# Kernel tuning notes

Hardware: AMD Instinct MI355X
Metric: run time of the kernel (lower is better)

The kernel has to match this reference:

```python
import jax, jax.numpy as jnp
import numpy as np

N, NFEAT, NHID, NHEADS, NCLASS, NBLOCKS = 4096, 1024, 64, 8, 8, 3
ALPHA = 0.1       # LeakyReLU negative slope
NEG = -9e15       # mask value used by pyGAT


def setup_inputs() -> dict:
    key = jax.random.key(0)
    ks = jax.random.split(key, 8)
    x = jax.random.normal(ks[0], (N, NFEAT), jnp.float32)
    # sparse-ish symmetric adjacency with self loops (0/1 int mask)
    a = (jax.random.uniform(ks[1], (N, N)) < 0.01).astype(jnp.int32)
    adj = jnp.maximum(jnp.maximum(a, a.T), jnp.eye(N, dtype=jnp.int32))
    s = 0.1
    W_heads = (jax.random.normal(ks[2], (NHEADS, NFEAT, NHID), jnp.float32) * s)
    a_heads = (jax.random.normal(ks[3], (NHEADS, 2 * NHID), jnp.float32) * s)
    W_out = (jax.random.normal(ks[4], (NHEADS * NHID, NHID), jnp.float32) * s)
    a_out = (jax.random.normal(ks[5], (2 * NHID,), jnp.float32) * s)
    W_gcn = (jax.random.normal(ks[6], (NBLOCKS, NHID, NHID), jnp.float32) * s)
    W_cls = (jax.random.normal(ks[7], (NHID, NCLASS), jnp.float32) * s)
    return dict(x=x, adj=adj, W_heads=W_heads, a_heads=a_heads,
                W_out=W_out, a_out=a_out, W_gcn=W_gcn, W_cls=W_cls)


def _gat_layer(h, mask, W, a, concat):
    # classic pyGAT dense GraphAttentionLayer (inference: dropout off)
    Wh = h @ W                      # [N, nhid]
    nh = Wh.shape[1]
    f1 = Wh @ a[:nh]                # [N]
    f2 = Wh @ a[nh:]                # [N]
    e = jax.nn.leaky_relu(f1[:, None] + f2[None, :], ALPHA)  # [N, N]
    att = jax.nn.softmax(jnp.where(mask, e, NEG), axis=1)
    hp = att @ Wh                   # [N, nhid]
    return jax.nn.elu(hp) if concat else hp


def reference(x, adj, W_heads, a_heads, W_out, a_out, W_gcn, W_cls):
    mask = adj > 0
    # multi-head GAT, concat heads (loop over small fixed head count to keep
    # peak memory at one [N,N] score matrix per step)
    heads = [_gat_layer(x, mask, W_heads[i], a_heads[i], True)
             for i in range(NHEADS)]
    h = jnp.concatenate(heads, axis=1)           # [N, nheads*nhid]
    h = _gat_layer(h, mask, W_out, a_out, False)  # [N, nhid]
    # ModifiedGCN: symmetric-normalized dense propagation, n_blocks + head
    af = adj.astype(h.dtype)
    dinv = jax.lax.rsqrt(jnp.sum(af, axis=1))
    a_norm = af * dinv[:, None] * dinv[None, :]   # D^-1/2 A D^-1/2
    for i in range(NBLOCKS):
        h = jax.nn.relu(a_norm @ (h @ W_gcn[i]))
    return a_norm @ (h @ W_cls)                   # [N, nclass]
```

## Files before the change

### kernel.cpp

```cpp
#include <hip/hip_runtime.h>
#include <hip/hip_bf16.h>
#include <math.h>

#define N_NODES 4096
#define NFEAT   1024
#define NHEADS  8
#define ALPHA   0.1f
#define MAXDEG  256

typedef short short8 __attribute__((ext_vector_type(8)));
typedef float f32x4  __attribute__((ext_vector_type(4)));

__device__ __forceinline__ ushort f2bf(float f) {
    uint b = __float_as_uint(f);
    b += 0x7FFFu + ((b >> 16) & 1u);
    return (ushort)(b >> 16);
}
__device__ __forceinline__ float bf2f(ushort u) {
    return __uint_as_float(((uint)u) << 16);
}

__global__ __launch_bounds__(256) void prep_all(const float* __restrict__ x,
                                                const int* __restrict__ adj,
                                                const float* __restrict__ Whd,
                                                const float* __restrict__ Wo,
                                                short* __restrict__ x3,
                                                short* __restrict__ W3,
                                                short* __restrict__ W23,
                                                ushort* __restrict__ csr,
                                                int* __restrict__ rowlen,
                                                float* __restrict__ dinv) {
    __shared__ float tile[64][65];
    int b = blockIdx.x, t = threadIdx.x;
    if (b < 4096) {
        size_t idx = ((size_t)b * 256 + t) * 4;
        int row = (int)(idx >> 10);
        int col = (int)(idx & 1023);
        float4 v = *(const float4*)(x + idx);
        ushort h0 = f2bf(v.x), h1 = f2bf(v.y), h2 = f2bf(v.z), h3 = f2bf(v.w);
        short4 h = make_short4((short)h0, (short)h1, (short)h2, (short)h3);
        short4 l = make_short4((short)f2bf(v.x - bf2f(h0)), (short)f2bf(v.y - bf2f(h1)),
                               (short)f2bf(v.z - bf2f(h2)), (short)f2bf(v.w - bf2f(h3)));
        short* rp = x3 + (size_t)row * 3072 + col;
        *(short4*)(rp)        = h;
        *(short4*)(rp + 1024) = l;
        *(short4*)(rp + 2048) = h;
        return;
    }
    if (b < 4232) {
        const float* W; short* B3; int K, head, kb;
        if (b < 4224) { int id = b - 4096; W = Whd; B3 = W3;  K = 1024; head = id >> 4; kb = id & 15; }
        else          { int id = b - 4224; W = Wo;  B3 = W23; K = 512;  head = 0;       kb = id; }
        int k0 = kb * 64;
        const float* src = W + (size_t)head * K * 64 + (size_t)k0 * 64;
#pragma unroll
        for (int i = 0; i < 16; i++) {
            int lin = t + i * 256;
            int kk = lin >> 6, nn = lin & 63;
            tile[nn][kk] = src[kk * 64 + nn];
        }
        __syncthreads();
#pragma unroll
        for (int i = 0; i < 16; i++) {
            int lin = t + i * 256;
            int nn = lin >> 6, kk = lin & 63;
            float v = tile[nn][kk];
            ushort h = f2bf(v);
            ushort l = f2bf(v - bf2f(h));
            short* rp = B3 + (size_t)(head * 64 + nn) * (3 * (size_t)K) + k0 + kk;
            rp[0]     = (short)h;
            rp[K]     = (short)h;
            rp[2 * K] = (short)l;
        }
        return;
    }
    int wid = t >> 6, lane = t & 63;
    int row = (b - 4232) * 4 + wid;
    const int4* arow = (const int4*)(adj + (size_t)row * N_NODES);
    unsigned long long pre = (1ull << lane) - 1ull;
    int count = 0;
    ushort* crow = csr + (size_t)row * MAXDEG;
    for (int blk = 0; blk < N_NODES / 256; blk++) {
        int4 v = arow[blk * 64 + lane];
        unsigned long long m0 = __ballot(v.x != 0);
        unsigned long long m1 = __ballot(v.y != 0);
        unsigned long long m2 = __ballot(v.z != 0);
        unsigned long long m3 = __ballot(v.w != 0);
        int pos = count + __popcll(m0 & pre) + __popcll(m1 & pre)
                        + __popcll(m2 & pre) + __popcll(m3 & pre);
        int base = blk * 256 + lane * 4;
        if (v.x) { if (pos < MAXDEG) crow[pos] = (ushort)base;       pos++; }
        if (v.y) { if (pos < MAXDEG) crow[pos] = (ushort)(base + 1); pos++; }
        if (v.z) { if (pos < MAXDEG) crow[pos] = (ushort)(base + 2); pos++; }
        if (v.w) { if (pos < MAXDEG) crow[pos] = (ushort)(base + 3); pos++; }
        count += __popcll(m0) + __popcll(m1) + __popcll(m2) + __popcll(m3);
    }
    if (lane == 0) {
        rowlen[row] = count < MAXDEG ? count : MAXDEG;
        dinv[row] = 1.0f / sqrtf((float)count);
    }
}

#define GBM 64
#define GBN 64
#define GBK 64
#define LDK 72

__global__ __launch_bounds__(256, 2) void gemm_mfma(const short* __restrict__ A,
                                                    const short* __restrict__ B,
                                                    float* __restrict__ C,
                                                    int Kp, int kChunk, int cPartStride,
                                                    int swz, int headmajor,
                                                    const float* __restrict__ aH,
                                                    float* __restrict__ f1h,
                                                    float* __restrict__ f2h) {
    __shared__ __align__(16) short As[2][GBM * LDK];
    __shared__ __align__(16) short Bs[2][GBN * LDK];

    int tid = threadIdx.x, lane = tid & 63, wid = tid >> 6;
    int wr = wid >> 1, wc = wid & 1;
    int bx, by;
    if (swz) {
        int lin = blockIdx.x;
        bx = (lin & 7) * 8 + (lin >> 6);
        by = (lin >> 3) & 7;
    } else {
        bx = blockIdx.x; by = blockIdx.y;
    }
    int row0 = bx * GBM, col0 = by * GBN;
    int kbase = blockIdx.z * kChunk;
    C += (size_t)blockIdx.z * cPartStride;

    int aRow[2], aKc[2], bRow[2], bKc[2];
#pragma unroll
    for (int c = 0; c < 2; c++) {
        int lin = tid + c * 256;
        aRow[c] = lin >> 3; aKc[c] = (lin & 7) * 8;
        bRow[c] = lin >> 3; bKc[c] = (lin & 7) * 8;
    }

    short8 rA[2], rB[2];
    auto LOAD = [&](int k0) {
#pragma unroll
        for (int c = 0; c < 2; c++) {
            rA[c] = *(const short8*)(A + (size_t)(row0 + aRow[c]) * Kp + kbase + k0 + aKc[c]);
            rB[c] = *(const short8*)(B + (size_t)(col0 + bRow[c]) * Kp + kbase + k0 + bKc[c]);
        }
    };
    auto WRITE = [&](int buf) {
#pragma unroll
        for (int c = 0; c < 2; c++) {
            *(short8*)&As[buf][aRow[c] * LDK + aKc[c]] = rA[c];
            *(short8*)&Bs[buf][bRow[c] * LDK + bKc[c]] = rB[c];
        }
    };

    f32x4 acc[2][2];
#pragma unroll
    for (int m = 0; m < 2; m++)
#pragma unroll
        for (int n = 0; n < 2; n++) acc[m][n] = (f32x4){0.f, 0.f, 0.f, 0.f};

    LOAD(0);
    WRITE(0);
    __syncthreads();

    int nt = kChunk / GBK;
    for (int t = 0; t < nt; ++t) {
        int cur = t & 1;
        if (t + 1 < nt) LOAD((t + 1) * GBK);
#pragma unroll
        for (int ks = 0; ks < 2; ++ks) {
            short8 ah[2], bh[2];
            int ko = ks * 32 + (lane >> 4) * 8;
#pragma unroll
            for (int m = 0; m < 2; m++)
                ah[m] = *(const short8*)&As[cur][(wr * 32 + m * 16 + (lane & 15)) * LDK + ko];
#pragma unroll
            for (int n = 0; n < 2; n++)
                bh[n] = *(const short8*)&Bs[cur][(wc * 32 + n * 16 + (lane & 15)) * LDK + ko];
#pragma unroll
            for (int m = 0; m < 2; m++)
#pragma unroll
                for (int n = 0; n < 2; n++)
                    acc[m][n] = __builtin_amdgcn_mfma_f32_16x16x32_bf16(ah[m], bh[n], acc[m][n], 0, 0, 0);
        }
        if (t + 1 < nt) WRITE(cur ^ 1);
        __syncthreads();
    }

#pragma unroll
    for (int m = 0; m < 2; m++)
#pragma unroll
        for (int n = 0; n < 2; n++)
#pragma unroll
            for (int r = 0; r < 4; r++) {
                int rr = row0 + wr * 32 + m * 16 + (lane >> 4) * 4 + r;
                int cc = col0 + wc * 32 + n * 16 + (lane & 15);
                if (headmajor)
                    C[(size_t)(cc >> 6) * (N_NODES * 64) + (size_t)rr * 64 + (cc & 63)] = acc[m][n][r];
                else
                    C[(size_t)rr * 64 + cc] = acc[m][n][r];
            }

    if (aH) {
        __shared__ float f1p[2][64], f2p[2][64];
        const float* ahp = aH + by * 128;
        int cl = lane & 15;
        float a1x = ahp[wc * 32 + cl],      a1y = ahp[wc * 32 + 16 + cl];
        float a2x = ahp[64 + wc * 32 + cl], a2y = ahp[64 + wc * 32 + 16 + cl];
#pragma unroll
        for (int m = 0; m < 2; m++)
#pragma unroll
            for (int r = 0; r < 4; r++) {
                float s1 = acc[m][0][r] * a1x + acc[m][1][r] * a1y;
                float s2 = acc[m][0][r] * a2x + acc[m][1][r] * a2y;
#pragma unroll
                for (int off = 1; off < 16; off <<= 1) {
                    s1 += __shfl_xor(s1, off);
                    s2 += __shfl_xor(s2, off);
                }
                if ((lane & 15) == 0) {
                    int rl = wr * 32 + m * 16 + (lane >> 4) * 4 + r;
                    f1p[wc][rl] = s1;
                    f2p[wc][rl] = s2;
                }
            }
        __syncthreads();
        if (tid < 64) {
            f1h[(size_t)by * N_NODES + row0 + tid] = f1p[0][tid] + f1p[1][tid];
            f2h[(size_t)by * N_NODES + row0 + tid] = f2p[0][tid] + f2p[1][tid];
        }
    }
}

__global__ __launch_bounds__(512, 8) void attn1(const float* __restrict__ Whh,
                                                const float* __restrict__ f1h,
                                                const float* __restrict__ f2h,
                                                const ushort* __restrict__ csr,
                                                const int* __restrict__ rowlen,
                                                short* __restrict__ hp3) {
    __shared__ float  f2s[N_NODES];
    __shared__ float  w[8][MAXDEG];
    __shared__ ushort cols[8][MAXDEG];
    int lin = blockIdx.x;
    int h = lin & 7;
    int wid = threadIdx.x >> 6, lane = threadIdx.x & 63;
    int i = (lin >> 3) * 8 + wid;

    {
        const float4* f2g = (const float4*)(f2h + (size_t)h * N_NODES);
        float4 v0 = f2g[threadIdx.x];
        float4 v1 = f2g[threadIdx.x + 512];
        *(float4*)&f2s[threadIdx.x * 4] = v0;
        *(float4*)&f2s[(threadIdx.x + 512) * 4] = v1;
    }
    __syncthreads();

    int len = rowlen[i];
    const ushort* crow = csr + (size_t)i * MAXDEG;
    float f1v = f1h[(size_t)h * N_NODES + i];

    float ev[4]; int cv[4];
    float m = -1e30f;
#pragma unroll
    for (int c = 0; c < 4; c++) {
        int k = lane + c * 64;
        if (k < len) {
            int j = crow[k];
            float e = f1v + f2s[j];
            e = e > 0.f ? e : ALPHA * e;
            ev[c] = e; cv[c] = j;
            m = fmaxf(m, e);
        }
    }
#pragma unroll
    for (int off = 32; off; off >>= 1) m = fmaxf(m, __shfl_xor(m, off));
    float s = 0.f;
#pragma unroll
    for (int c = 0; c < 4; c++) {
        int k = lane + c * 64;
        if (k < len) {
            float ex = __expf(ev[c] - m);
            s += ex;
            w[wid][k] = ex;
            cols[wid][k] = (ushort)cv[c];
        }
    }
#pragma unroll
    for (int off = 32; off; off >>= 1) s += __shfl_xor(s, off);
    float sinv = 1.0f / s;

    int len16 = (len + 15) & ~15;
    if (lane < len16 - len) {
        w[wid][len + lane] = 0.f;
        cols[wid][len + lane] = 0;
    }

    int q = lane >> 4, d = lane & 15;
    const float4* base = (const float4*)(Whh + (size_t)h * (N_NODES * 64)) + d;
    f32x4 A0 = {0.f,0.f,0.f,0.f}, A1 = A0, A2 = A0, A3 = A0;
    for (int k = 0; k < len16; k += 16) {
        int   j0 = cols[wid][k + q];       float w0 = w[wid][k + q];
        int   j1 = cols[wid][k + 4 + q];   float w1 = w[wid][k + 4 + q];
        int   j2 = cols[wid][k + 8 + q];   float w2 = w[wid][k + 8 + q];
        int   j3 = cols[wid][k + 12 + q];  float w3 = w[wid][k + 12 + q];
        float4 v0 = base[(size_t)j0 * 16];
        float4 v1 = base[(size_t)j1 * 16];
        float4 v2 = base[(size_t)j2 * 16];
        float4 v3 = base[(size_t)j3 * 16];
        A0[0] += w0 * v0.x; A0[1] += w0 * v0.y; A0[2] += w0 * v0.z; A0[3] += w0 * v0.w;
        A1[0] += w1 * v1.x; A1[1] += w1 * v1.y; A1[2] += w1 * v1.z; A1[3] += w1 * v1.w;
        A2[0] += w2 * v2.x; A2[1] += w2 * v2.y; A2[2] += w2 * v2.z; A2[3] += w2 * v2.w;
        A3[0] += w3 * v3.x; A3[1] += w3 * v3.y; A3[2] += w3 * v3.z; A3[3] += w3 * v3.w;
    }
    float rx = (A0[0] + A1[0]) + (A2[0] + A3[0]);
    float ry = (A0[1] + A1[1]) + (A2[1] + A3[1]);
    float rz = (A0[2] + A1[2]) + (A2[2] + A3[2]);
    float rw = (A0[3] + A1[3]) + (A2[3] + A3[3]);
#pragma unroll
    for (int off = 16; off <= 32; off <<= 1) {
        rx += __shfl_xor(rx, off);
        ry += __shfl_xor(ry, off);
        rz += __shfl_xor(rz, off);
        rw += __shfl_xor(rw, off);
    }
    if (lane < 16) {
        float v[4] = {rx * sinv, ry * sinv, rz * sinv, rw * sinv};
        short hi[4], lo[4];
#pragma unroll
        for (int c = 0; c < 4; c++) {
            float e = v[c] > 0.f ? v[c] : __expf(v[c]) - 1.f;
            ushort hh = f2bf(e);
            hi[c] = (short)hh;
            lo[c] = (short)f2bf(e - bf2f(hh));
        }
        short* rp = hp3 + (size_t)i * 1536 + h * 64 + d * 4;
        *(short4*)(rp)        = make_short4(hi[0], hi[1], hi[2], hi[3]);
        *(short4*)(rp + 512)  = make_short4(lo[0], lo[1], lo[2], lo[3]);
        *(short4*)(rp + 1024) = make_short4(hi[0], hi[1], hi[2], hi[3]);
    }
}

__global__ __launch_bounds__(256) void f2sum(const float* __restrict__ part,
                                             const float* __restrict__ a,
                                             float* __restrict__ Wh2,
                                             float* __restrict__ f1o,
                                             float* __restrict__ f2o) {
    int wid = threadIdx.x >> 6, l = threadIdx.x & 63;
    int i = blockIdx.x * 4 + wid;
    size_t o = (size_t)i * 64 + l;
    const size_t S = (size_t)N_NODES * 64;
    float v = part[o] + part[o + S] + part[o + 2 * S] + part[o + 3 * S];
    Wh2[o] = v;
    float p1 = v * a[l], p2 = v * a[64 + l];
#pragma unroll
    for (int off = 32; off; off >>= 1) {
        p1 += __shfl_xor(p1, off);
        p2 += __shfl_xor(p2, off);
    }
    if (l == 0) { f1o[i] = p1; f2o[i] = p2; }
}

__global__ __launch_bounds__(256, 6) void attn2_g0(const float* __restrict__ Wh2,
                                                   const float* __restrict__ f1o,
                                                   const float* __restrict__ f2o,
                                                   const ushort* __restrict__ csr,
                                                   const int* __restrict__ rowlen,
                                                   const float* __restrict__ W0,
                                                   const float* __restrict__ dinv,
                                                   float* __restrict__ t0) {
    __shared__ float  f2s[N_NODES];
    __shared__ float  w[4][MAXDEG];
    __shared__ ushort cl[4][MAXDEG];
    __shared__ float  hrow[4][64];
    int wid = threadIdx.x >> 6, lane = threadIdx.x & 63;
    int i = blockIdx.x * 4 + wid;

    {
        const float4* f2g = (const float4*)f2o;
#pragma unroll
        for (int c = 0; c < 4; c++) {
            int idx = threadIdx.x + c * 256;
            *(float4*)&f2s[idx * 4] = f2g[idx];
        }
    }
    __syncthreads();

    int len = rowlen[i];
    const ushort* crow = csr + (size_t)i * MAXDEG;
    float myf1 = f1o[i];

    float ev[4]; int cv[4];
    float m = -1e30f;
#pragma unroll
    for (int c = 0; c < 4; c++) {
        int k = lane + c * 64;
        if (k < len) {
            int j = crow[k];
            float e = myf1 + f2s[j];
            e = e > 0.f ? e : ALPHA * e;
            ev[c] = e; cv[c] = j;
            m = fmaxf(m, e);
        }
    }
#pragma unroll
    for (int off = 32; off; off >>= 1) m = fmaxf(m, __shfl_xor(m, off));
    float s = 0.f;
#pragma unroll
    for (int c = 0; c < 4; c++) {
        int k = lane + c * 64;
        if (k < len) {
            float ex = __expf(ev[c] - m);
            s += ex;
            w[wid][k] = ex;
            cl[wid][k] = (ushort)cv[c];
        }
    }
#pragma unroll
    for (int off = 32; off; off >>= 1) s += __shfl_xor(s, off);
    float sinv = 1.0f / s;

    int len16 = (len + 15) & ~15;
    if (lane < len16 - len) {
        w[wid][len + lane] = 0.f;
        cl[wid][len + lane] = 0;
    }

    int q = lane >> 4, d = lane & 15;
    const float4* base = (const float4*)Wh2 + d;
    f32x4 A0 = {0.f,0.f,0.f,0.f}, A1 = A0, A2 = A0, A3 = A0;
    for (int k = 0; k < len16; k += 16) {
        int   j0 = cl[wid][k + q];       float w0 = w[wid][k + q];
        int   j1 = cl[wid][k + 4 + q];   float w1 = w[wid][k + 4 + q];
        int   j2 = cl[wid][k + 8 + q];   float w2 = w[wid][k + 8 + q];
        int   j3 = cl[wid][k + 12 + q];  float w3 = w[wid][k + 12 + q];
        float4 v0 = base[(size_t)j0 * 16];
        float4 v1 = base[(size_t)j1 * 16];
        float4 v2 = base[(size_t)j2 * 16];
        float4 v3 = base[(size_t)j3 * 16];
        A0[0] += w0 * v0.x; A0[1] += w0 * v0.y; A0[2] += w0 * v0.z; A0[3] += w0 * v0.w;
        A1[0] += w1 * v1.x; A1[1] += w1 * v1.y; A1[2] += w1 * v1.z; A1[3] += w1 * v1.w;
        A2[0] += w2 * v2.x; A2[1] += w2 * v2.y; A2[2] += w2 * v2.z; A2[3] += w2 * v2.w;
        A3[0] += w3 * v3.x; A3[1] += w3 * v3.y; A3[2] += w3 * v3.z; A3[3] += w3 * v3.w;
    }
    float rx = (A0[0] + A1[0]) + (A2[0] + A3[0]);
    float ry = (A0[1] + A1[1]) + (A2[1] + A3[1]);
    float rz = (A0[2] + A1[2]) + (A2[2] + A3[2]);
    float rw = (A0[3] + A1[3]) + (A2[3] + A3[3]);
#pragma unroll
    for (int off = 16; off <= 32; off <<= 1) {
        rx += __shfl_xor(rx, off);
        ry += __shfl_xor(ry, off);
        rz += __shfl_xor(rz, off);
        rw += __shfl_xor(rw, off);
    }
    if (lane < 16) {
        float4 r = make_float4(rx * sinv, ry * sinv, rz * sinv, rw * sinv);
        *(float4*)&hrow[wid][d * 4] = r;
    }

    float ox = 0.f, oy = 0.f, oz = 0.f, ow = 0.f;
#pragma unroll
    for (int it = 0; it < 16; it++) {
        int kk = q * 16 + it;
        float hv = hrow[wid][kk];
        float4 wv = *(const float4*)(W0 + kk * 64 + d * 4);
        ox += hv * wv.x; oy += hv * wv.y; oz += hv * wv.z; ow += hv * wv.w;
    }
#pragma unroll
    for (int off = 16; off <= 32; off <<= 1) {
        ox += __shfl_xor(ox, off);
        oy += __shfl_xor(oy, off);
        oz += __shfl_xor(oz, off);
        ow += __shfl_xor(ow, off);
    }
    if (lane < 16) {
        float di = dinv[i];
        *(float4*)(t0 + (size_t)i * 64 + d * 4) =
            make_float4(ox * di, oy * di, oz * di, ow * di);
    }
}

__global__ __launch_bounds__(256, 4) void spmv_gemm(const float* __restrict__ t,
                                                    const ushort* __restrict__ csr,
                                                    const int* __restrict__ rowlen,
                                                    const float* __restrict__ W,
                                                    const float* __restrict__ dinv,
                                                    float* __restrict__ out) {
    __shared__ float hrow[4][64];
    int wid = threadIdx.x >> 6, lane = threadIdx.x & 63;
    int i = blockIdx.x * 4 + wid;
    int len = rowlen[i];
    const ushort* ci = csr + (size_t)i * MAXDEG;
    int q = lane >> 4, d = lane & 15;
    const float4* base = (const float4*)t + d;
    int len16 = (len + 15) & ~15;
    f32x4 A0 = {0.f,0.f,0.f,0.f}, A1 = A0, A2 = A0, A3 = A0;
    for (int k = 0; k < len16; k += 16) {
        int k0 = k + q, k1 = k + 4 + q, k2 = k + 8 + q, k3 = k + 12 + q;
        float m0 = k0 < len ? 1.f : 0.f;
        float m1 = k1 < len ? 1.f : 0.f;
        float m2 = k2 < len ? 1.f : 0.f;
        float m3 = k3 < len ? 1.f : 0.f;
        int j0 = ci[k0 < len ? k0 : 0];
        int j1 = ci[k1 < len ? k1 : 0];
        int j2 = ci[k2 < len ? k2 : 0];
        int j3 = ci[k3 < len ? k3 : 0];
        float4 v0 = base[(size_t)j0 * 16];
        float4 v1 = base[(size_t)j1 * 16];
        float4 v2 = base[(size_t)j2 * 16];
        float4 v3 = base[(size_t)j3 * 16];
        A0[0] += m0 * v0.x; A0[1] += m0 * v0.y; A0[2] += m0 * v0.z; A0[3] += m0 * v0.w;
        A1[0] += m1 * v1.x; A1[1] += m1 * v1.y; A1[2] += m1 * v1.z; A1[3] += m1 * v1.w;
        A2[0] += m2 * v2.x; A2[1] += m2 * v2.y; A2[2] += m2 * v2.z; A2[3] += m2 * v2.w;
        A3[0] += m3 * v3.x; A3[1] += m3 * v3.y; A3[2] += m3 * v3.z; A3[3] += m3 * v3.w;
    }
    float rx = (A0[0] + A1[0]) + (A2[0] + A3[0]);
    float ry = (A0[1] + A1[1]) + (A2[1] + A3[1]);
    float rz = (A0[2] + A1[2]) + (A2[2] + A3[2]);
    float rw = (A0[3] + A1[3]) + (A2[3] + A3[3]);
#pragma unroll
    for (int off = 16; off <= 32; off <<= 1) {
        rx += __shfl_xor(rx, off);
        ry += __shfl_xor(ry, off);
        rz += __shfl_xor(rz, off);
        rw += __shfl_xor(rw, off);
    }
    float di = dinv[i];
    if (lane < 16) {
        float4 r = make_float4(fmaxf(rx * di, 0.f), fmaxf(ry * di, 0.f),
                               fmaxf(rz * di, 0.f), fmaxf(rw * di, 0.f));
        *(float4*)&hrow[wid][d * 4] = r;
    }

    float ox = 0.f, oy = 0.f, oz = 0.f, ow = 0.f;
#pragma unroll
    for (int it = 0; it < 16; it++) {
        int kk = q * 16 + it;
        float hv = hrow[wid][kk];
        float4 wv = *(const float4*)(W + kk * 64 + d * 4);
        ox += hv * wv.x; oy += hv * wv.y; oz += hv * wv.z; ow += hv * wv.w;
    }
#pragma unroll
    for (int off = 16; off <= 32; off <<= 1) {
        ox += __shfl_xor(ox, off);
        oy += __shfl_xor(oy, off);
        oz += __shfl_xor(oz, off);
        ow += __shfl_xor(ow, off);
    }
    if (lane < 16)
        *(float4*)(out + (size_t)i * 64 + d * 4) =
            make_float4(ox * di, oy * di, oz * di, ow * di);
}

__global__ __launch_bounds__(256, 4) void spmv_cls(const float* __restrict__ t,
                                                   const ushort* __restrict__ csr,
                                                   const int* __restrict__ rowlen,
                                                   const float* __restrict__ Wc,
                                                   const float* __restrict__ dinv,
                                                   float* __restrict__ t8) {
    __shared__ float hrow[4][64];
    int wid = threadIdx.x >> 6, lane = threadIdx.x & 63;
    int i = blockIdx.x * 4 + wid;
    int len = rowlen[i];
    const ushort* ci = csr + (size_t)i * MAXDEG;
    int q = lane >> 4, d = lane & 15;
    const float4* base = (const float4*)t + d;
    int len16 = (len + 15) & ~15;
    f32x4 A0 = {0.f,0.f,0.f,0.f}, A1 = A0, A2 = A0, A3 = A0;
    for (int k = 0; k < len16; k += 16) {
        int k0 = k + q, k1 = k + 4 + q, k2 = k + 8 + q, k3 = k + 12 + q;
        float m0 = k0 < len ? 1.f : 0.f;
        float m1 = k1 < len ? 1.f : 0.f;
        float m2 = k2 < len ? 1.f : 0.f;
        float m3 = k3 < len ? 1.f : 0.f;
        int j0 = ci[k0 < len ? k0 : 0];
        int j1 = ci[k1 < len ? k1 : 0];
        int j2 = ci[k2 < len ? k2 : 0];
        int j3 = ci[k3 < len ? k3 : 0];
        float4 v0 = base[(size_t)j0 * 16];
        float4 v1 = base[(size_t)j1 * 16];
        float4 v2 = base[(size_t)j2 * 16];
        float4 v3 = base[(size_t)j3 * 16];
        A0[0] += m0 * v0.x; A0[1] += m0 * v0.y; A0[2] += m0 * v0.z; A0[3] += m0 * v0.w;
        A1[0] += m1 * v1.x; A1[1] += m1 * v1.y; A1[2] += m1 * v1.z; A1[3] += m1 * v1.w;
        A2[0] += m2 * v2.x; A2[1] += m2 * v2.y; A2[2] += m2 * v2.z; A2[3] += m2 * v2.w;
        A3[0] += m3 * v3.x; A3[1] += m3 * v3.y; A3[2] += m3 * v3.z; A3[3] += m3 * v3.w;
    }
    float rx = (A0[0] + A1[0]) + (A2[0] + A3[0]);
    float ry = (A0[1] + A1[1]) + (A2[1] + A3[1]);
    float rz = (A0[2] + A1[2]) + (A2[2] + A3[2]);
    float rw = (A0[3] + A1[3]) + (A2[3] + A3[3]);
#pragma unroll
    for (int off = 16; off <= 32; off <<= 1) {
        rx += __shfl_xor(rx, off);
        ry += __shfl_xor(ry, off);
        rz += __shfl_xor(rz, off);
        rw += __shfl_xor(rw, off);
    }
    float di = dinv[i];
    if (lane < 16) {
        float4 r = make_float4(fmaxf(rx * di, 0.f), fmaxf(ry * di, 0.f),
                               fmaxf(rz * di, 0.f), fmaxf(rw * di, 0.f));
        *(float4*)&hrow[wid][d * 4] = r;
    }
    int col = lane & 7, k0s = (lane >> 3) * 8;
    float o = 0.f;
#pragma unroll
    for (int kk = 0; kk < 8; kk++) o += hrow[wid][k0s + kk] * Wc[(k0s + kk) * 8 + col];
    o += __shfl_down(o, 32);
    o += __shfl_down(o, 16);
    o += __shfl_down(o, 8);
    if (lane < 8) t8[(size_t)i * 8 + lane] = o * di;
}

__global__ __launch_bounds__(256) void spmv8(const float* __restrict__ t8,
                                             const ushort* __restrict__ csr,
                                             const int* __restrict__ rowlen,
                                             const float* __restrict__ dinv,
                                             float* __restrict__ out) {
    int wid = threadIdx.x >> 6, lane = threadIdx.x & 63;
    int i = blockIdx.x * 4 + wid;
    int len = rowlen[i];
    const ushort* ci = csr + (size_t)i * MAXDEG;
    int col = lane & 7, chunk = lane >> 3;
    float acc = 0.f;
    for (int k = chunk; k < len; k += 8)
        acc += t8[(size_t)ci[k] * 8 + col];
    acc += __shfl_down(acc, 32);
    acc += __shfl_down(acc, 16);
    acc += __shfl_down(acc, 8);
    if (lane < 8) out[(size_t)i * 8 + lane] = acc * dinv[i];
}

extern "C" void kernel_launch(void* const* d_in, const int* in_sizes, int n_in,
                              void* d_out, int out_size, void* d_ws, size_t ws_size,
                              hipStream_t stream) {
    const float* x       = (const float*)d_in[0];
    const int*   adj     = (const int*)d_in[1];
    const float* W_heads = (const float*)d_in[2];
    const float* a_heads = (const float*)d_in[3];
    const float* W_out   = (const float*)d_in[4];
    const float* a_out   = (const float*)d_in[5];
    const float* W_gcn   = (const float*)d_in[6];
    const float* W_cls   = (const float*)d_in[7];
    float* outp = (float*)d_out;

    char* p = (char*)d_ws;
    short*  x3     = (short*)p;  p += (size_t)N_NODES * 3072 * 2;
    short*  W3     = (short*)p;  p += (size_t)512 * 3072 * 2;
    short*  W23    = (short*)p;  p += (size_t)64 * 1536 * 2;
    float*  Whh    = (float*)p;  p += (size_t)NHEADS * N_NODES * 64 * 4;
    float*  f1h    = (float*)p;  p += (size_t)NHEADS * N_NODES * 4;
    float*  f2h    = (float*)p;  p += (size_t)NHEADS * N_NODES * 4;
    float*  Wh2    = (float*)p;  p += (size_t)N_NODES * 64 * 4;
    float*  f1o    = (float*)p;  p += (size_t)N_NODES * 4;
    float*  f2o    = (float*)p;  p += (size_t)N_NODES * 4;
    float*  tA     = (float*)p;  p += (size_t)N_NODES * 64 * 4;
    float*  tB     = (float*)p;  p += (size_t)N_NODES * 64 * 4;
    float*  t8     = (float*)p;  p += (size_t)N_NODES * 8 * 4;
    float*  dinv   = (float*)p;  p += (size_t)N_NODES * 4;
    int*    rowlen = (int*)p;    p += (size_t)N_NODES * 4;
    ushort* csr    = (ushort*)p; p += (size_t)N_NODES * MAXDEG * 2;

    short* hp3  = x3;
    float* part = (float*)((char*)x3 + (16u << 20));

    prep_all<<<4096 + 128 + 8 + 1024, 256, 0, stream>>>(
        x, adj, W_heads, W_out, x3, W3, W23, csr, rowlen, dinv);

    gemm_mfma<<<512, 256, 0, stream>>>(x3, W3, Whh, 3072, 3072, 0, 1, 1,
                                       a_heads, f1h, f2h);

    attn1<<<N_NODES * NHEADS / 8, 512, 0, stream>>>(Whh, f1h, f2h, csr, rowlen, hp3);

    gemm_mfma<<<dim3(N_NODES / GBM, 1, 4), 256, 0, stream>>>(
        hp3, W23, part, 1536, 384, N_NODES * 64, 0, 0, nullptr, nullptr, nullptr);

    f2sum<<<N_NODES / 4, 256, 0, stream>>>(part, a_out, Wh2, f1o, f2o);

    attn2_g0<<<N_NODES / 4, 256, 0, stream>>>(Wh2, f1o, f2o, csr, rowlen, W_gcn, dinv, tA);

    spmv_gemm<<<N_NODES / 4, 256, 0, stream>>>(tA, csr, rowlen, W_gcn + 4096, dinv, tB);
    spmv_gemm<<<N_NODES / 4, 256, 0, stream>>>(tB, csr, rowlen, W_gcn + 8192, dinv, tA);

    spmv_cls<<<N_NODES / 4, 256, 0, stream>>>(tA, csr, rowlen, W_cls, dinv, t8);
    spmv8<<<N_NODES / 4, 256, 0, stream>>>(t8, csr, rowlen, dinv, outp);
}
```

Before: 245.1 us.

## Deepen GEMM K tile and software-pipeline gather loops in attention and SpMV kernels

The MFMA GEMM K tile doubles from 64 to 128 (LDS stride 136), so each thread loads four 16-byte chunks per operand and there are fewer barrier-separated iterations. The gather loops in attn1, the second attention kernel and spmv_gemm are software-pipelined: the next 16 neighbour rows are prefetched into registers while the current ones are accumulated. The last prefetch reads index 0 harmlessly. Launch-bound occupancy hints change (attn1 8→6, spmv_gemm 4→6). This trades more registers and LDS for better latency hiding.

```diff
diff --git a/kernel.cpp b/kernel.cpp
--- a/kernel.cpp
+++ b/kernel.cpp
@@ -103,8 +103,8 @@
 
 #define GBM 64
 #define GBN 64
-#define GBK 64
-#define LDK 72
+#define GBK 128
+#define LDK 136
 
 __global__ __launch_bounds__(256, 2) void gemm_mfma(const short* __restrict__ A,
                                                     const short* __restrict__ B,
@@ -131,27 +131,26 @@
     int kbase = blockIdx.z * kChunk;
     C += (size_t)blockIdx.z * cPartStride;
 
-    int aRow[2], aKc[2], bRow[2], bKc[2];
-#pragma unroll
-    for (int c = 0; c < 2; c++) {
+    int aRow[4], aKc[4];
+#pragma unroll
+    for (int c = 0; c < 4; c++) {
         int lin = tid + c * 256;
-        aRow[c] = lin >> 3; aKc[c] = (lin & 7) * 8;
-        bRow[c] = lin >> 3; bKc[c] = (lin & 7) * 8;
-    }
-
-    short8 rA[2], rB[2];
+        aRow[c] = lin >> 4; aKc[c] = (lin & 15) * 8;
+    }
+
+    short8 rA[4], rB[4];
     auto LOAD = [&](int k0) {
 #pragma unroll
-        for (int c = 0; c < 2; c++) {
+        for (int c = 0; c < 4; c++) {
             rA[c] = *(const short8*)(A + (size_t)(row0 + aRow[c]) * Kp + kbase + k0 + aKc[c]);
-            rB[c] = *(const short8*)(B + (size_t)(col0 + bRow[c]) * Kp + kbase + k0 + bKc[c]);
+            rB[c] = *(const short8*)(B + (size_t)(col0 + aRow[c]) * Kp + kbase + k0 + aKc[c]);
         }
     };
     auto WRITE = [&](int buf) {
 #pragma unroll
-        for (int c = 0; c < 2; c++) {
+        for (int c = 0; c < 4; c++) {
             *(short8*)&As[buf][aRow[c] * LDK + aKc[c]] = rA[c];
-            *(short8*)&Bs[buf][bRow[c] * LDK + bKc[c]] = rB[c];
+            *(short8*)&Bs[buf][aRow[c] * LDK + aKc[c]] = rB[c];
         }
     };
 
@@ -170,7 +169,7 @@
         int cur = t & 1;
         if (t + 1 < nt) LOAD((t + 1) * GBK);
 #pragma unroll
-        for (int ks = 0; ks < 2; ++ks) {
+        for (int ks = 0; ks < GBK / 32; ++ks) {
             short8 ah[2], bh[2];
             int ko = ks * 32 + (lane >> 4) * 8;
 #pragma unroll
@@ -234,7 +233,7 @@
     }
 }
 
-__global__ __launch_bounds__(512, 8) void attn1(const float* __restrict__ Whh,
+__global__ __launch_bounds__(512, 6) void attn1(const float* __restrict__ Whh,
                                                 const float* __restrict__ f1h,
                                                 const float* __restrict__ f2h,
                                                 const ushort* __restrict__ csr,
@@ -300,20 +299,36 @@
     int q = lane >> 4, d = lane & 15;
     const float4* base = (const float4*)(Whh + (size_t)h * (N_NODES * 64)) + d;
     f32x4 A0 = {0.f,0.f,0.f,0.f}, A1 = A0, A2 = A0, A3 = A0;
-    for (int k = 0; k < len16; k += 16) {
-        int   j0 = cols[wid][k + q];       float w0 = w[wid][k + q];
-        int   j1 = cols[wid][k + 4 + q];   float w1 = w[wid][k + 4 + q];
-        int   j2 = cols[wid][k + 8 + q];   float w2 = w[wid][k + 8 + q];
-        int   j3 = cols[wid][k + 12 + q];  float w3 = w[wid][k + 12 + q];
-        float4 v0 = base[(size_t)j0 * 16];
-        float4 v1 = base[(size_t)j1 * 16];
-        float4 v2 = base[(size_t)j2 * 16];
-        float4 v3 = base[(size_t)j3 * 16];
+
+    int   j0 = cols[wid][q],      j1 = cols[wid][4 + q];
+    int   j2 = cols[wid][8 + q],  j3 = cols[wid][12 + q];
+    float w0 = w[wid][q],         w1 = w[wid][4 + q];
+    float w2 = w[wid][8 + q],     w3 = w[wid][12 + q];
+    float4 v0 = base[(size_t)j0 * 16];
+    float4 v1 = base[(size_t)j1 * 16];
+    float4 v2 = base[(size_t)j2 * 16];
+    float4 v3 = base[(size_t)j3 * 16];
+
+    for (int k = 16; k <= len16; k += 16) {
+        int kk = (k < len16) ? k : 0;
+        int   n0 = cols[wid][kk + q],      n1 = cols[wid][kk + 4 + q];
+        int   n2 = cols[wid][kk + 8 + q],  n3 = cols[wid][kk + 12 + q];
+        float u0 = w[wid][kk + q],         u1 = w[wid][kk + 4 + q];
+        float u2 = w[wid][kk + 8 + q],     u3 = w[wid][kk + 12 + q];
+        float4 p0 = base[(size_t)n0 * 16];
+        float4 p1 = base[(size_t)n1 * 16];
+        float4 p2 = base[(size_t)n2 * 16];
+        float4 p3 = base[(size_t)n3 * 16];
+
         A0[0] += w0 * v0.x; A0[1] += w0 * v0.y; A0[2] += w0 * v0.z; A0[3] += w0 * v0.w;
         A1[0] += w1 * v1.x; A1[1] += w1 * v1.y; A1[2] += w1 * v1.z; A1[3] += w1 * v1.w;
         A2[0] += w2 * v2.x; A2[1] += w2 * v2.y; A2[2] += w2 * v2.z; A2[3] += w2 * v2.w;
         A3[0] += w3 * v3.x; A3[1] += w3 * v3.y; A3[2] += w3 * v3.z; A3[3] += w3 * v3.w;
-    }
+
+        w0 = u0; w1 = u1; w2 = u2; w3 = u3;
+        v0 = p0; v1 = p1; v2 = p2; v3 = p3;
+    }
+
     float rx = (A0[0] + A1[0]) + (A2[0] + A3[0]);
     float ry = (A0[1] + A1[1]) + (A2[1] + A3[1]);
     float rz = (A0[2] + A1[2]) + (A2[2] + A3[2]);
@@ -430,19 +445,34 @@
     int q = lane >> 4, d = lane & 15;
     const float4* base = (const float4*)Wh2 + d;
     f32x4 A0 = {0.f,0.f,0.f,0.f}, A1 = A0, A2 = A0, A3 = A0;
-    for (int k = 0; k < len16; k += 16) {
-        int   j0 = cl[wid][k + q];       float w0 = w[wid][k + q];
-        int   j1 = cl[wid][k + 4 + q];   float w1 = w[wid][k + 4 + q];
-        int   j2 = cl[wid][k + 8 + q];   float w2 = w[wid][k + 8 + q];
-        int   j3 = cl[wid][k + 12 + q];  float w3 = w[wid][k + 12 + q];
-        float4 v0 = base[(size_t)j0 * 16];
-        float4 v1 = base[(size_t)j1 * 16];
-        float4 v2 = base[(size_t)j2 * 16];
-        float4 v3 = base[(size_t)j3 * 16];
+
+    int   j0 = cl[wid][q],      j1 = cl[wid][4 + q];
+    int   j2 = cl[wid][8 + q],  j3 = cl[wid][12 + q];
+    float w0 = w[wid][q],       w1 = w[wid][4 + q];
+    float w2 = w[wid][8 + q],   w3 = w[wid][12 + q];
+    float4 v0 = base[(size_t)j0 * 16];
+    float4 v1 = base[(size_t)j1 * 16];
+    float4 v2 = base[(size_t)j2 * 16];
+    float4 v3 = base[(size_t)j3 * 16];
+
+    for (int k = 16; k <= len16; k += 16) {
+        int kk = (k < len16) ? k : 0;
+        int   n0 = cl[wid][kk + q],      n1 = cl[wid][kk + 4 + q];
+        int   n2 = cl[wid][kk + 8 + q],  n3 = cl[wid][kk + 12 + q];
+        float u0 = w[wid][kk + q],       u1 = w[wid][kk + 4 + q];
+        float u2 = w[wid][kk + 8 + q],   u3 = w[wid][kk + 12 + q];
+        float4 p0 = base[(size_t)n0 * 16];
+        float4 p1 = base[(size_t)n1 * 16];
+        float4 p2 = base[(size_t)n2 * 16];
+        float4 p3 = base[(size_t)n3 * 16];
+
         A0[0] += w0 * v0.x; A0[1] += w0 * v0.y; A0[2] += w0 * v0.z; A0[3] += w0 * v0.w;
         A1[0] += w1 * v1.x; A1[1] += w1 * v1.y; A1[2] += w1 * v1.z; A1[3] += w1 * v1.w;
         A2[0] += w2 * v2.x; A2[1] += w2 * v2.y; A2[2] += w2 * v2.z; A2[3] += w2 * v2.w;
         A3[0] += w3 * v3.x; A3[1] += w3 * v3.y; A3[2] += w3 * v3.z; A3[3] += w3 * v3.w;
+
+        w0 = u0; w1 = u1; w2 = u2; w3 = u3;
+        v0 = p0; v1 = p1; v2 = p2; v3 = p3;
     }
     float rx = (A0[0] + A1[0]) + (A2[0] + A3[0]);
     float ry = (A0[1] + A1[1]) + (A2[1] + A3[1]);
@@ -482,7 +512,7 @@
     }
 }
 
-__global__ __launch_bounds__(256, 4) void spmv_gemm(const float* __restrict__ t,
+__global__ __launch_bounds__(256, 6) void spmv_gemm(const float* __restrict__ t,
                                                     const ushort* __restrict__ csr,
                                                     const int* __restrict__ rowlen,
                                                     const float* __restrict__ W,
@@ -497,24 +527,44 @@
     const float4* base = (const float4*)t + d;
     int len16 = (len + 15) & ~15;
     f32x4 A0 = {0.f,0.f,0.f,0.f}, A1 = A0, A2 = A0, A3 = A0;
-    for (int k = 0; k < len16; k += 16) {
-        int k0 = k + q, k1 = k + 4 + q, k2 = k + 8 + q, k3 = k + 12 + q;
-        float m0 = k0 < len ? 1.f : 0.f;
-        float m1 = k1 < len ? 1.f : 0.f;
-        float m2 = k2 < len ? 1.f : 0.f;
-        float m3 = k3 < len ? 1.f : 0.f;
-        int j0 = ci[k0 < len ? k0 : 0];
-        int j1 = ci[k1 < len ? k1 : 0];
-        int j2 = ci[k2 < len ? k2 : 0];
-        int j3 = ci[k3 < len ? k3 : 0];
-        float4 v0 = base[(size_t)j0 * 16];
-        float4 v1 = base[(size_t)j1 * 16];
-        float4 v2 = base[(size_t)j2 * 16];
-        float4 v3 = base[(size_t)j3 * 16];
-        A0[0] += m0 * v0.x; A0[1] += m0 * v0.y; A0[2] += m0 * v0.z; A0[3] += m0 * v0.w;
-        A1[0] += m1 * v1.x; A1[1] += m1 * v1.y; A1[2] += m1 * v1.z; A1[3] += m1 * v1.w;
-        A2[0] += m2 * v2.x; A2[1] += m2 * v2.y; A2[2] += m2 * v2.z; A2[3] += m2 * v2.w;
-        A3[0] += m3 * v3.x; A3[1] += m3 * v3.y; A3[2] += m3 * v3.z; A3[3] += m3 * v3.w;
+
+    int k0 = q, k1 = 4 + q, k2 = 8 + q, k3 = 12 + q;
+    float w0 = k0 < len ? 1.f : 0.f;
+    float w1 = k1 < len ? 1.f : 0.f;
+    float w2 = k2 < len ? 1.f : 0.f;
+    float w3 = k3 < len ? 1.f : 0.f;
+    int j0 = ci[k0 < len ? k0 : 0];
+    int j1 = ci[k1 < len ? k1 : 0];
+    int j2 = ci[k2 < len ? k2 : 0];
+    int j3 = ci[k3 < len ? k3 : 0];
+    float4 v0 = base[(size_t)j0 * 16];
+    float4 v1 = base[(size_t)j1 * 16];
+    float4 v2 = base[(size_t)j2 * 16];
+    float4 v3 = base[(size_t)j3 * 16];
+
+    for (int k = 16; k <= len16; k += 16) {
+        int kk = (k < len16) ? k : 0;
+        int K0 = kk + q, K1 = kk + 4 + q, K2 = kk + 8 + q, K3 = kk + 12 + q;
+        float u0 = K0 < len ? 1.f : 0.f;
+        float u1 = K1 < len ? 1.f : 0.f;
+        float u2 = K2 < len ? 1.f : 0.f;
+        float u3 = K3 < len ? 1.f : 0.f;
+        int n0 = ci[K0 < len ? K0 : 0];
+        int n1 = ci[K1 < len ? K1 : 0];
+        int n2 = ci[K2 < len ? K2 : 0];
+        int n3 = ci[K3 < len ? K3 : 0];
+        float4 p0 = base[(size_t)n0 * 16];
+        float4 p1 = base[(size_t)n1 * 16];
+        float4 p2 = base[(size_t)n2 * 16];
+        float4 p3 = base[(size_t)n3 * 16];
+
+        A0[0] += w0 * v0.x; A0[1] += w0 * v0.y; A0[2] += w0 * v0.z; A0[3] += w0 * v0.w;
+        A1[0] += w1 * v1.x; A1[1] += w1 * v1.y; A1[2] += w1 * v1.z; A1[3] += w1 * v1.w;
+        A2[0] += w2 * v2.x; A2[1] += w2 * v2.y; A2[2] += w2 * v2.z; A2[3] += w2 * v2.w;
+        A3[0] += w3 * v3.x; A3[1] += w3 * v3.y; A3[2] += w3 * v3.z; A3[3] += w3 * v3.w;
+
+        w0 = u0; w1 = u1; w2 = u2; w3 = u3;
+        v0 = p0; v1 = p1; v2 = p2; v3 = p3;
     }
     float rx = (A0[0] + A1[0]) + (A2[0] + A3[0]);
     float ry = (A0[1] + A1[1]) + (A2[1] + A3[1]);
```

Measured after the change: 243.3 us. Within noise of the previous version (-0.8%).

## Add dedicated 128-row GEMM with direct LDS loads, two rows per wave in attn1

Applied to the files above, without the earlier changes.

Adds a dedicated first-layer GEMM with 128x64 tiles. It stages A and B straight into LDS with global_load_lds and keeps the fused f1/f2 attention projection epilogue. The generic gemm_mfma loses its head-major and fused-projection paths and moves to a K tile of 128 (LDK 136) for the second GEMM. attn1 now processes two rows per wave with 8-wide padding, and spmv_gemm's launch bound moves to 6 waves. The aim is more reuse per tile, fewer register round-trips for staging, and more memory-level parallelism in the gather. The cost is higher LDS use, which may lower occupancy, especially in attn1.

```diff
diff --git a/kernel.cpp b/kernel.cpp
--- a/kernel.cpp
+++ b/kernel.cpp
@@ -101,57 +101,155 @@
     }
 }
 
+__global__ __launch_bounds__(256) void gemm1_m97(const short* __restrict__ A,
+                                                 const short* __restrict__ B,
+                                                 float* __restrict__ C,
+                                                 const float* __restrict__ aH,
+                                                 float* __restrict__ f1h,
+                                                 float* __restrict__ f2h) {
+    __shared__ __align__(16) short As[2][128 * 64];
+    __shared__ __align__(16) short Bs[2][64 * 64];
+    __shared__ float f1p[2][128], f2p[2][128];
+
+    int tid = threadIdx.x, lane = tid & 63, wid = tid >> 6;
+    int wr = wid >> 1, wc = wid & 1;
+    int lin = blockIdx.x;
+    int bx = (lin & 7) * 4 + (lin >> 6);
+    int by = (lin >> 3) & 7;
+    int row0 = bx * 128, col0 = by * 64;
+    const int Kp = 3072;
+
+    int sRow = lane >> 3;
+    int sCol = (lane & 7) * 8;
+
+    auto STAGE = [&](int buf, int k0) {
+#pragma unroll
+        for (int c = 0; c < 4; c++) {
+            int q = c * 4 + wid;
+            const short* gp = A + (size_t)(row0 + 8 * q + sRow) * Kp + k0 + sCol;
+            __builtin_amdgcn_global_load_lds(
+                (const __attribute__((address_space(1))) void*)gp,
+                (__attribute__((address_space(3))) void*)&As[buf][q * 512], 16, 0, 0);
+        }
+#pragma unroll
+        for (int c = 0; c < 2; c++) {
+            int q = c * 4 + wid;
+            const short* gp = B + (size_t)(col0 + 8 * q + sRow) * Kp + k0 + sCol;
+            __builtin_amdgcn_global_load_lds(
+                (const __attribute__((address_space(1))) void*)gp,
+                (__attribute__((address_space(3))) void*)&Bs[buf][q * 512], 16, 0, 0);
+        }
+    };
+
+    f32x4 acc[4][2];
+#pragma unroll
+    for (int m = 0; m < 4; m++)
+#pragma unroll
+        for (int n = 0; n < 2; n++) acc[m][n] = (f32x4){0.f, 0.f, 0.f, 0.f};
+
+    STAGE(0, 0);
+    __syncthreads();
+
+    const int nt = 48;
+    for (int t = 0; t < nt; ++t) {
+        int cur = t & 1;
+        if (t + 1 < nt) STAGE(cur ^ 1, (t + 1) * 64);
+#pragma unroll
+        for (int ks = 0; ks < 2; ++ks) {
+            short8 ah[4], bh[2];
+            int ko = ks * 32 + (lane >> 4) * 8;
+#pragma unroll
+            for (int m = 0; m < 4; m++)
+                ah[m] = *(const short8*)&As[cur][(wr * 64 + m * 16 + (lane & 15)) * 64 + ko];
+#pragma unroll
+            for (int n = 0; n < 2; n++)
+                bh[n] = *(const short8*)&Bs[cur][(wc * 32 + n * 16 + (lane & 15)) * 64 + ko];
+#pragma unroll
+            for (int m = 0; m < 4; m++)
+#pragma unroll
+                for (int n = 0; n < 2; n++)
+                    acc[m][n] = __builtin_amdgcn_mfma_f32_16x16x32_bf16(ah[m], bh[n], acc[m][n], 0, 0, 0);
+        }
+        __syncthreads();
+    }
+
+#pragma unroll
+    for (int m = 0; m < 4; m++)
+#pragma unroll
+        for (int n = 0; n < 2; n++)
+#pragma unroll
+            for (int r = 0; r < 4; r++) {
+                int rr = row0 + wr * 64 + m * 16 + (lane >> 4) * 4 + r;
+                int cc = wc * 32 + n * 16 + (lane & 15);
+                C[(size_t)by * (N_NODES * 64) + (size_t)rr * 64 + cc] = acc[m][n][r];
+            }
+
+    const float* ahp = aH + by * 128;
+    int cl = lane & 15;
+    float a1x = ahp[wc * 32 + cl],      a1y = ahp[wc * 32 + 16 + cl];
+    float a2x = ahp[64 + wc * 32 + cl], a2y = ahp[64 + wc * 32 + 16 + cl];
+#pragma unroll
+    for (int m = 0; m < 4; m++)
+#pragma unroll
+        for (int r = 0; r < 4; r++) {
+            float s1 = acc[m][0][r] * a1x + acc[m][1][r] * a1y;
+            float s2 = acc[m][0][r] * a2x + acc[m][1][r] * a2y;
+#pragma unroll
+            for (int off = 1; off < 16; off <<= 1) {
+                s1 += __shfl_xor(s1, off);
+                s2 += __shfl_xor(s2, off);
+            }
+            if ((lane & 15) == 0) {
+                int rl = wr * 64 + m * 16 + (lane >> 4) * 4 + r;
+                f1p[wc][rl] = s1;
+                f2p[wc][rl] = s2;
+            }
+        }
+    __syncthreads();
+    if (tid < 128) {
+        f1h[(size_t)by * N_NODES + row0 + tid] = f1p[0][tid] + f1p[1][tid];
+        f2h[(size_t)by * N_NODES + row0 + tid] = f2p[0][tid] + f2p[1][tid];
+    }
+}
+
 #define GBM 64
 #define GBN 64
-#define GBK 64
-#define LDK 72
+#define GBK 128
+#define LDK 136
 
 __global__ __launch_bounds__(256, 2) void gemm_mfma(const short* __restrict__ A,
                                                     const short* __restrict__ B,
                                                     float* __restrict__ C,
-                                                    int Kp, int kChunk, int cPartStride,
-                                                    int swz, int headmajor,
-                                                    const float* __restrict__ aH,
-                                                    float* __restrict__ f1h,
-                                                    float* __restrict__ f2h) {
+                                                    int Kp, int kChunk, int cPartStride) {
     __shared__ __align__(16) short As[2][GBM * LDK];
     __shared__ __align__(16) short Bs[2][GBN * LDK];
 
     int tid = threadIdx.x, lane = tid & 63, wid = tid >> 6;
     int wr = wid >> 1, wc = wid & 1;
-    int bx, by;
-    if (swz) {
-        int lin = blockIdx.x;
-        bx = (lin & 7) * 8 + (lin >> 6);
-        by = (lin >> 3) & 7;
-    } else {
-        bx = blockIdx.x; by = blockIdx.y;
-    }
-    int row0 = bx * GBM, col0 = by * GBN;
+    int row0 = blockIdx.x * GBM, col0 = blockIdx.y * GBN;
     int kbase = blockIdx.z * kChunk;
     C += (size_t)blockIdx.z * cPartStride;
 
-    int aRow[2], aKc[2], bRow[2], bKc[2];
-#pragma unroll
-    for (int c = 0; c < 2; c++) {
+    int aRow[4], aKc[4];
+#pragma unroll
+    for (int c = 0; c < 4; c++) {
         int lin = tid + c * 256;
-        aRow[c] = lin >> 3; aKc[c] = (lin & 7) * 8;
-        bRow[c] = lin >> 3; bKc[c] = (lin & 7) * 8;
-    }
-
-    short8 rA[2], rB[2];
+        aRow[c] = lin >> 4; aKc[c] = (lin & 15) * 8;
+    }
+
+    short8 rA[4], rB[4];
     auto LOAD = [&](int k0) {
 #pragma unroll
-        for (int c = 0; c < 2; c++) {
+        for (int c = 0; c < 4; c++) {
             rA[c] = *(const short8*)(A + (size_t)(row0 + aRow[c]) * Kp + kbase + k0 + aKc[c]);
-            rB[c] = *(const short8*)(B + (size_t)(col0 + bRow[c]) * Kp + kbase + k0 + bKc[c]);
+            rB[c] = *(const short8*)(B + (size_t)(col0 + aRow[c]) * Kp + kbase + k0 + aKc[c]);
         }
     };
     auto WRITE = [&](int buf) {
 #pragma unroll
-        for (int c = 0; c < 2; c++) {
+        for (int c = 0; c < 4; c++) {
             *(short8*)&As[buf][aRow[c] * LDK + aKc[c]] = rA[c];
-            *(short8*)&Bs[buf][bRow[c] * LDK + bKc[c]] = rB[c];
+            *(short8*)&Bs[buf][aRow[c] * LDK + aKc[c]] = rB[c];
         }
     };
 
@@ -170,7 +268,7 @@
         int cur = t & 1;
         if (t + 1 < nt) LOAD((t + 1) * GBK);
 #pragma unroll
-        for (int ks = 0; ks < 2; ++ks) {
+        for (int ks = 0; ks < GBK / 32; ++ks) {
             short8 ah[2], bh[2];
             int ko = ks * 32 + (lane >> 4) * 8;
 #pragma unroll
@@ -197,56 +295,24 @@
             for (int r = 0; r < 4; r++) {
                 int rr = row0 + wr * 32 + m * 16 + (lane >> 4) * 4 + r;
                 int cc = col0 + wc * 32 + n * 16 + (lane & 15);
-                if (headmajor)
-                    C[(size_t)(cc >> 6) * (N_NODES * 64) + (size_t)rr * 64 + (cc & 63)] = acc[m][n][r];
-                else
-                    C[(size_t)rr * 64 + cc] = acc[m][n][r];
+                C[(size_t)rr * 64 + cc] = acc[m][n][r];
             }
-
-    if (aH) {
-        __shared__ float f1p[2][64], f2p[2][64];
-        const float* ahp = aH + by * 128;
-        int cl = lane & 15;
-        float a1x = ahp[wc * 32 + cl],      a1y = ahp[wc * 32 + 16 + cl];
-        float a2x = ahp[64 + wc * 32 + cl], a2y = ahp[64 + wc * 32 + 16 + cl];
-#pragma unroll
-        for (int m = 0; m < 2; m++)
-#pragma unroll
-            for (int r = 0; r < 4; r++) {
-                float s1 = acc[m][0][r] * a1x + acc[m][1][r] * a1y;
-                float s2 = acc[m][0][r] * a2x + acc[m][1][r] * a2y;
-#pragma unroll
-                for (int off = 1; off < 16; off <<= 1) {
-                    s1 += __shfl_xor(s1, off);
-                    s2 += __shfl_xor(s2, off);
-                }
-                if ((lane & 15) == 0) {
-                    int rl = wr * 32 + m * 16 + (lane >> 4) * 4 + r;
-                    f1p[wc][rl] = s1;
-                    f2p[wc][rl] = s2;
-                }
-            }
-        __syncthreads();
-        if (tid < 64) {
-            f1h[(size_t)by * N_NODES + row0 + tid] = f1p[0][tid] + f1p[1][tid];
-            f2h[(size_t)by * N_NODES + row0 + tid] = f2p[0][tid] + f2p[1][tid];
-        }
-    }
-}
-
-__global__ __launch_bounds__(512, 8) void attn1(const float* __restrict__ Whh,
+}
+
+__global__ __launch_bounds__(512, 4) void attn1(const float* __restrict__ Whh,
                                                 const float* __restrict__ f1h,
                                                 const float* __restrict__ f2h,
                                                 const ushort* __restrict__ csr,
                                                 const int* __restrict__ rowlen,
                                                 short* __restrict__ hp3) {
     __shared__ float  f2s[N_NODES];
-    __shared__ float  w[8][MAXDEG];
-    __shared__ ushort cols[8][MAXDEG];
+    __shared__ float  w[16][MAXDEG];
+    __shared__ ushort cols[16][MAXDEG];
     int lin = blockIdx.x;
     int h = lin & 7;
     int wid = threadIdx.x >> 6, lane = threadIdx.x & 63;
-    int i = (lin >> 3) * 8 + wid;
+    int i0 = (lin >> 3) * 16 + wid * 2;
+    int sA = wid * 2, sB = sA + 1;
 
     {
         const float4* f2g = (const float4*)(f2h + (size_t)h * N_NODES);
@@ -257,88 +323,98 @@
     }
     __syncthreads();
 
-    int len = rowlen[i];
-    const ushort* crow = csr + (size_t)i * MAXDEG;
-    float f1v = f1h[(size_t)h * N_NODES + i];
-
-    float ev[4]; int cv[4];
-    float m = -1e30f;
-#pragma unroll
-    for (int c = 0; c < 4; c++) {
-        int k = lane + c * 64;
-        if (k < len) {
-            int j = crow[k];
-            float e = f1v + f2s[j];
-            e = e > 0.f ? e : ALPHA * e;
-            ev[c] = e; cv[c] = j;
-            m = fmaxf(m, e);
-        }
-    }
-#pragma unroll
-    for (int off = 32; off; off >>= 1) m = fmaxf(m, __shfl_xor(m, off));
-    float s = 0.f;
-#pragma unroll
-    for (int c = 0; c < 4; c++) {
-        int k = lane + c * 64;
-        if (k < len) {
-            float ex = __expf(ev[c] - m);
-            s += ex;
-            w[wid][k] = ex;
-            cols[wid][k] = (ushort)cv[c];
-        }
-    }
-#pragma unroll
-    for (int off = 32; off; off >>= 1) s += __shfl_xor(s, off);
-    float sinv = 1.0f / s;
-
-    int len16 = (len + 15) & ~15;
-    if (lane < len16 - len) {
-        w[wid][len + lane] = 0.f;
-        cols[wid][len + lane] = 0;
-    }
+    float sinvR[2];
+    int lenR[2];
+#pragma unroll
+    for (int r = 0; r < 2; r++) {
+        int i = i0 + r, slot = sA + r;
+        int len = rowlen[i];
+        lenR[r] = len;
+        const ushort* crow = csr + (size_t)i * MAXDEG;
+        float f1v = f1h[(size_t)h * N_NODES + i];
+        float ev[4]; int cv[4];
+        float m = -1e30f;
+#pragma unroll
+        for (int c = 0; c < 4; c++) {
+            int k = lane + c * 64;
+            if (k < len) {
+                int j = crow[k];
+                float e = f1v + f2s[j];
+                e = e > 0.f ? e : ALPHA * e;
+                ev[c] = e; cv[c] = j;
+                m = fmaxf(m, e);
+            }
+        }
+#pragma unroll
+        for (int off = 32; off; off >>= 1) m = fmaxf(m, __shfl_xor(m, off));
+        float s = 0.f;
+#pragma unroll
+        for (int c = 0; c < 4; c++) {
+            int k = lane + c * 64;
+            if (k < len) {
+                float ex = __expf(ev[c] - m);
+                s += ex;
+                w[slot][k] = ex;
+                cols[slot][k] = (ushort)cv[c];
+            }
+        }
+#pragma unroll
+        for (int off = 32; off; off >>= 1) s += __shfl_xor(s, off);
+        sinvR[r] = 1.0f / s;
+    }
+
+    int lc = lenR[0] > lenR[1] ? lenR[0] : lenR[1];
+    int len8 = (lc + 7) & ~7;
+    for (int k = lenR[0] + lane; k < len8; k += 64) { w[sA][k] = 0.f; cols[sA][k] = 0; }
+    for (int k = lenR[1] + lane; k < len8; k += 64) { w[sB][k] = 0.f; cols[sB][k] = 0; }
 
     int q = lane >> 4, d = lane & 15;
     const float4* base = (const float4*)(Whh + (size_t)h * (N_NODES * 64)) + d;
-    f32x4 A0 = {0.f,0.f,0.f,0.f}, A1 = A0, A2 = A0, A3 = A0;
-    for (int k = 0; k < len16; k += 16) {
-        int   j0 = cols[wid][k + q];       float w0 = w[wid][k + q];
-        int   j1 = cols[wid][k + 4 + q];   float w1 = w[wid][k + 4 + q];
-        int   j2 = cols[wid][k + 8 + q];   float w2 = w[wid][k + 8 + q];
-        int   j3 = cols[wid][k + 12 + q];  float w3 = w[wid][k + 12 + q];
-        float4 v0 = base[(size_t)j0 * 16];
-        float4 v1 = base[(size_t)j1 * 16];
-        float4 v2 = base[(size_t)j2 * 16];
-        float4 v3 = base[(size_t)j3 * 16];
-        A0[0] += w0 * v0.x; A0[1] += w0 * v0.y; A0[2] += w0 * v0.z; A0[3] += w0 * v0.w;
-        A1[0] += w1 * v1.x; A1[1] += w1 * v1.y; A1[2] += w1 * v1.z; A1[3] += w1 * v1.w;
-        A2[0] += w2 * v2.x; A2[1] += w2 * v2.y; A2[2] += w2 * v2.z; A2[3] += w2 * v2.w;
-        A3[0] += w3 * v3.x; A3[1] += w3 * v3.y; A3[2] += w3 * v3.z; A3[3] += w3 * v3.w;
-    }
-    float rx = (A0[0] + A1[0]) + (A2[0] + A3[0]);
-    float ry = (A0[1] + A1[1]) + (A2[1] + A3[1]);
-    float rz = (A0[2] + A1[2]) + (A2[2] + A3[2]);
-    float rw = (A0[3] + A1[3]) + (A2[3] + A3[3]);
-#pragma unroll
-    for (int off = 16; off <= 32; off <<= 1) {
-        rx += __shfl_xor(rx, off);
-        ry += __shfl_xor(ry, off);
-        rz += __shfl_xor(rz, off);
-        rw += __shfl_xor(rw, off);
-    }
-    if (lane < 16) {
-        float v[4] = {rx * sinv, ry * sinv, rz * sinv, rw * sinv};
-        short hi[4], lo[4];
-#pragma unroll
-        for (int c = 0; c < 4; c++) {
-            float e = v[c] > 0.f ? v[c] : __expf(v[c]) - 1.f;
-            ushort hh = f2bf(e);
-            hi[c] = (short)hh;
-            lo[c] = (short)f2bf(e - bf2f(hh));
-        }
-        short* rp = hp3 + (size_t)i * 1536 + h * 64 + d * 4;
-        *(short4*)(rp)        = make_short4(hi[0], hi[1], hi[2], hi[3]);
-        *(short4*)(rp + 512)  = make_short4(lo[0], lo[1], lo[2], lo[3]);
-        *(short4*)(rp + 1024) = make_short4(hi[0], hi[1], hi[2], hi[3]);
+    f32x4 A0 = {0.f,0.f,0.f,0.f}, A1 = A0, B0 = A0, B1 = A0;
+    for (int k = 0; k < len8; k += 8) {
+        int   ja0 = cols[sA][k + q];      float wa0 = w[sA][k + q];
+        int   ja1 = cols[sA][k + 4 + q];  float wa1 = w[sA][k + 4 + q];
+        int   jb0 = cols[sB][k + q];      float wb0 = w[sB][k + q];
+        int   jb1 = cols[sB][k + 4 + q];  float wb1 = w[sB][k + 4 + q];
+        float4 va0 = base[(size_t)ja0 * 16];
+        float4 va1 = base[(size_t)ja1 * 16];
+        float4 vb0 = base[(size_t)jb0 * 16];
+        float4 vb1 = base[(size_t)jb1 * 16];
+        A0[0] += wa0 * va0.x; A0[1] += wa0 * va0.y; A0[2] += wa0 * va0.z; A0[3] += wa0 * va0.w;
+        A1[0] += wa1 * va1.x; A1[1] += wa1 * va1.y; A1[2] += wa1 * va1.z; A1[3] += wa1 * va1.w;
+        B0[0] += wb0 * vb0.x; B0[1] += wb0 * vb0.y; B0[2] += wb0 * vb0.z; B0[3] += wb0 * vb0.w;
+        B1[0] += wb1 * vb1.x; B1[1] += wb1 * vb1.y; B1[2] += wb1 * vb1.z; B1[3] += wb1 * vb1.w;
+    }
+
+#pragma unroll
+    for (int r = 0; r < 2; r++) {
+        f32x4 R;
+        if (r == 0) { R[0]=A0[0]+A1[0]; R[1]=A0[1]+A1[1]; R[2]=A0[2]+A1[2]; R[3]=A0[3]+A1[3]; }
+        else        { R[0]=B0[0]+B1[0]; R[1]=B0[1]+B1[1]; R[2]=B0[2]+B1[2]; R[3]=B0[3]+B1[3]; }
+        float rx = R[0], ry = R[1], rz = R[2], rw = R[3];
+#pragma unroll
+        for (int off = 16; off <= 32; off <<= 1) {
+            rx += __shfl_xor(rx, off);
+            ry += __shfl_xor(ry, off);
+            rz += __shfl_xor(rz, off);
+            rw += __shfl_xor(rw, off);
+        }
+        if (lane < 16) {
+            float sinv = sinvR[r];
+            float v[4] = {rx * sinv, ry * sinv, rz * sinv, rw * sinv};
+            short hi[4], lo[4];
+#pragma unroll
+            for (int c = 0; c < 4; c++) {
+                float e = v[c] > 0.f ? v[c] : __expf(v[c]) - 1.f;
+                ushort hh = f2bf(e);
+                hi[c] = (short)hh;
+                lo[c] = (short)f2bf(e - bf2f(hh));
+            }
+            short* rp = hp3 + (size_t)(i0 + r) * 1536 + h * 64 + d * 4;
+            *(short4*)(rp)        = make_short4(hi[0], hi[1], hi[2], hi[3]);
+            *(short4*)(rp + 512)  = make_short4(lo[0], lo[1], lo[2], lo[3]);
+            *(short4*)(rp + 1024) = make_short4(hi[0], hi[1], hi[2], hi[3]);
+        }
     }
 }
 
@@ -482,7 +558,7 @@
     }
 }
 
-__global__ __launch_bounds__(256, 4) void spmv_gemm(const float* __restrict__ t,
+__global__ __launch_bounds__(256, 6) void spmv_gemm(const float* __restrict__ t,
                                                     const ushort* __restrict__ csr,
                                                     const int* __restrict__ rowlen,
                                                     const float* __restrict__ W,
@@ -670,13 +746,12 @@
     prep_all<<<4096 + 128 + 8 + 1024, 256, 0, stream>>>(
         x, adj, W_heads, W_out, x3, W3, W23, csr, rowlen, dinv);
 
-    gemm_mfma<<<512, 256, 0, stream>>>(x3, W3, Whh, 3072, 3072, 0, 1, 1,
-                                       a_heads, f1h, f2h);
-
-    attn1<<<N_NODES * NHEADS / 8, 512, 0, stream>>>(Whh, f1h, f2h, csr, rowlen, hp3);
+    gemm1_m97<<<256, 256, 0, stream>>>(x3, W3, Whh, a_heads, f1h, f2h);
+
+    attn1<<<N_NODES * NHEADS / 16, 512, 0, stream>>>(Whh, f1h, f2h, csr, rowlen, hp3);
 
     gemm_mfma<<<dim3(N_NODES / GBM, 1, 4), 256, 0, stream>>>(
-        hp3, W23, part, 1536, 384, N_NODES * 64, 0, 0, nullptr, nullptr, nullptr);
+        hp3, W23, part, 1536, 384, N_NODES * 64);
 
     f2sum<<<N_NODES / 4, 256, 0, stream>>>(part, a_out, Wh2, f1o, f2o);
 
```

Measured after the change: 275.4 us. +12.4%, slower.
